# Kernel optimization log

Hardware: AMD Instinct MI355X
Metric: run time of the kernel (lower is better)

## Reference

```python
import jax, jax.numpy as jnp
import numpy as np

NODE_DIM = 128
HIDDEN = 64
N_NODES = 100000
N_REL = 50
N_EDGES = 1000000
TEMPERATURE = 0.5
BIAS = 1e-4


def _xavier(key, shape):
    fan_in, fan_out = shape[0], shape[1]
    lim = jnp.sqrt(6.0 / (fan_in + fan_out))
    return jax.random.uniform(key, shape, jnp.float32, -lim, lim)


def setup_inputs() -> dict:
    key = jax.random.key(0)
    ks = jax.random.split(key, 16)
    inp = {
        "edge_index": jax.random.randint(ks[0], (2, N_EDGES), 0, N_NODES),
        "edge_type": jax.random.randint(ks[1], (N_EDGES,), 0, N_REL),
        "all_embed": jax.random.normal(ks[2], (N_NODES, NODE_DIM), jnp.float32),
        "relation_emb": jax.random.normal(ks[3], (N_REL, NODE_DIM), jnp.float32),
        "u": jax.random.uniform(ks[4], (N_EDGES,), jnp.float32),
    }
    # four 2-layer MLPs: Linear(node_dim, hidden) -> ReLU -> Linear(hidden, 1)
    names = ["src", "dst", "edge", "con"]
    for i, nm in enumerate(names):
        k1, k2 = jax.random.split(ks[5 + i])
        inp[f"W1_{nm}"] = _xavier(k1, (NODE_DIM, HIDDEN))
        inp[f"b1_{nm}"] = jnp.zeros((HIDDEN,), jnp.float32)
        inp[f"W2_{nm}"] = _xavier(k2, (HIDDEN, 1))
        inp[f"b2_{nm}"] = jnp.zeros((1,), jnp.float32)
    return inp


def _mlp(x, W1, b1, W2, b2):
    # x: [E, node_dim] -> [E, 1]
    h = jnp.maximum(x @ W1 + b1, 0.0)
    return h @ W2 + b2


def reference(edge_index, edge_type, all_embed, relation_emb, u,
              W1_src, b1_src, W2_src, b2_src,
              W1_dst, b1_dst, W2_dst, b2_dst,
              W1_edge, b1_edge, W2_edge, b2_edge,
              W1_con, b1_con, W2_con, b2_con):
    head = all_embed[edge_index[0]]          # [E, D] gather
    tail = all_embed[edge_index[1]]          # [E, D] gather
    latent = relation_emb[edge_type]         # [E, D] gather

    weight = _mlp(head + tail + latent, W1_con, b1_con, W2_con, b2_con)
    weight = weight + _mlp(head, W1_src, b1_src, W2_src, b2_src)
    weight = weight + _mlp(tail, W1_dst, b1_dst, W2_dst, b2_dst)
    weight = weight + _mlp(latent, W1_edge, b1_edge, W2_edge, b2_edge)
    weight = weight[:, 0]                    # squeeze -> [E]

    # eps = (bias - (1-bias)) * u + (1-bias), bias = 1e-4
    eps = (2.0 * BIAS - 1.0) * u + (1.0 - BIAS)
    gate_inputs = jnp.log(eps) - jnp.log1p(-eps)
    gate_inputs = (gate_inputs + weight) / TEMPERATURE
    return jax.nn.sigmoid(gate_inputs)       # [E]
```

## Files before the change

### kernel.cpp

```cpp
#include <hip/hip_runtime.h>
#include <hip/hip_bf16.h>
#include <hip/hip_fp16.h>
#include <math.h>

#define NODE_DIM 128
#define HIDDEN   64
#define N_NODES  100000
#define N_RELS   50
#define N_EDGESC 1000000
#define TEMPERATURE 0.5f
#define BIASF 0.0001f
#define NBLK_GEMM ((N_NODES + 127) / 128)

typedef __attribute__((ext_vector_type(8))) _Float16 f16x8;
typedef __attribute__((ext_vector_type(2))) _Float16 hv2;
typedef __attribute__((ext_vector_type(4))) float    f32x4;

union U4 { uint4 u; hv2 h[4]; };

__global__ __launch_bounds__(256) void prep_small(
    const float* __restrict__ W1c, const float* __restrict__ W1s,
    const float* __restrict__ W1d,
    _Float16* __restrict__ wt) {
  const int tid = blockIdx.x * 256 + threadIdx.x;
  const int k = tid / 192;
  const int n = tid % 192;
  const float* W = (n < 64) ? W1c : (n < 128) ? W1s : W1d;
  const float v = W[k * HIDDEN + (n & 63)];
  const int ks = k ^ ((n & 7) << 3);
  wt[n * NODE_DIM + ks] = (_Float16)v;
}

__global__ __launch_bounds__(512) void prep_gemm(
    const float* __restrict__ x,
    const _Float16* __restrict__ wt,
    const float* __restrict__ b1s, const float* __restrict__ W2s,
    const float* __restrict__ b2s,
    const float* __restrict__ b1d, const float* __restrict__ W2d,
    const float* __restrict__ b2d,
    const float* __restrict__ rel_emb,
    const float* __restrict__ W1c, const float* __restrict__ b1c,
    const float* __restrict__ W1e, const float* __restrict__ b1e,
    const float* __restrict__ W2e, const float* __restrict__ b2e,
    const float* __restrict__ b2c, const float* __restrict__ W2c,
    __half* __restrict__ pcon,
    float* __restrict__ ssrc, float* __restrict__ sdst,
    _Float16* __restrict__ qh, float* __restrict__ srel,
    _Float16* __restrict__ w2h) {
  const int wv = threadIdx.x >> 6;
  const int l  = threadIdx.x & 63;

  if (blockIdx.x >= NBLK_GEMM) {
    if (blockIdx.x == NBLK_GEMM && threadIdx.x < HIDDEN)
      w2h[threadIdx.x] = (_Float16)W2c[threadIdx.x];
    const int r = (blockIdx.x - NBLK_GEMM) * 8 + wv;
    if (r >= N_RELS) return;
    const float* xr = rel_emb + (size_t)r * NODE_DIM;
    float ac = 0.f, ae = 0.f;
    #pragma unroll 8
    for (int k = 0; k < NODE_DIM; ++k) {
      float xk = xr[k];
      ac = fmaf(xk, W1c[k * HIDDEN + l], ac);
      ae = fmaf(xk, W1e[k * HIDDEN + l], ae);
    }
    qh[r * HIDDEN + l] = (_Float16)(ac + b1c[l]);
    float he = fmaxf(ae + b1e[l], 0.f) * W2e[l];
    #pragma unroll
    for (int off = 32; off > 0; off >>= 1) he += __shfl_xor(he, off);
    if (l == 0) srel[r] = he + b2e[0] + b2c[0];
    return;
  }

  __shared__ _Float16 bl[192 * NODE_DIM];
  const int hi = l >> 4;
  const int c  = l & 15;

  {
    const char* g = (const char*)wt;
    #pragma unroll
    for (int i = 0; i < 6; ++i) {
      const int chunk = (i * 8 + wv) << 10;
      __builtin_amdgcn_global_load_lds(
          (const __attribute__((address_space(1))) void*)(g + chunk + l * 16),
          (__attribute__((address_space(3))) void*)((char*)bl + chunk),
          16, 0, 0);
    }
  }

  const int m0   = blockIdx.x * 128 + wv * 16;
  const int arow = m0 + c;
  const int rowc = arow < N_NODES ? arow : N_NODES - 1;
  const float* xr = x + (size_t)rowc * NODE_DIM + hi * 8;
  f16x8 a[4];
  #pragma unroll
  for (int s = 0; s < 4; ++s) {
    float4 u0 = *(const float4*)(xr + s * 32);
    float4 u1 = *(const float4*)(xr + s * 32 + 4);
    f16x8 av;
    av[0] = (_Float16)u0.x; av[1] = (_Float16)u0.y;
    av[2] = (_Float16)u0.z; av[3] = (_Float16)u0.w;
    av[4] = (_Float16)u1.x; av[5] = (_Float16)u1.y;
    av[6] = (_Float16)u1.z; av[7] = (_Float16)u1.w;
    a[s] = av;
  }

  __syncthreads();

  f32x4 acc[12];
  #pragma unroll
  for (int i = 0; i < 12; ++i) acc[i] = (f32x4){0.f, 0.f, 0.f, 0.f};

  #pragma unroll
  for (int tt = 0; tt < 12; ++tt) {
    const int n = tt * 16 + c;
    const int nbase = n * NODE_DIM;
    #pragma unroll
    for (int s = 0; s < 4; ++s) {
      const int ks = (s * 32 + hi * 8) ^ ((n & 7) << 3);
      f16x8 b = *(const f16x8*)(&bl[nbase + ks]);
      acc[tt] = __builtin_amdgcn_mfma_f32_16x16x32_f16(a[s], b, acc[tt], 0, 0, 0);
    }
  }

  #pragma unroll
  for (int tt = 0; tt < 4; ++tt) {
    #pragma unroll
    for (int g = 0; g < 4; ++g) {
      const int row = m0 + hi * 4 + g;
      if (row < N_NODES)
        pcon[(size_t)row * HIDDEN + tt * 16 + c] = __float2half(acc[tt][g]);
    }
  }
  float ps[4] = {0.f, 0.f, 0.f, 0.f};
  float pd[4] = {0.f, 0.f, 0.f, 0.f};
  #pragma unroll
  for (int tt = 0; tt < 4; ++tt) {
    const int h = tt * 16 + c;
    const float b1sv = b1s[h], w2sv = W2s[h];
    const float b1dv = b1d[h], w2dv = W2d[h];
    #pragma unroll
    for (int g = 0; g < 4; ++g) {
      ps[g] += fmaxf(acc[4 + tt][g] + b1sv, 0.f) * w2sv;
      pd[g] += fmaxf(acc[8 + tt][g] + b1dv, 0.f) * w2dv;
    }
  }
  #pragma unroll
  for (int off = 1; off < 16; off <<= 1) {
    #pragma unroll
    for (int g = 0; g < 4; ++g) {
      ps[g] += __shfl_xor(ps[g], off);
      pd[g] += __shfl_xor(pd[g], off);
    }
  }
  if (c == 0) {
    const float bs = b2s[0], bd = b2d[0];
    #pragma unroll
    for (int g = 0; g < 4; ++g) {
      const int row = m0 + hi * 4 + g;
      if (row < N_NODES) { ssrc[row] = ps[g] + bs; sdst[row] = pd[g] + bd; }
    }
  }
}

__global__ __launch_bounds__(256) void edge_kernel(
    const int*   __restrict__ edge_index,
    const int*   __restrict__ edge_type,
    const float* __restrict__ u,
    const _Float16* __restrict__ pcon,
    const float* __restrict__ ssrc,
    const float* __restrict__ sdst,
    const _Float16* __restrict__ qh,
    const float* __restrict__ srel,
    const _Float16* __restrict__ w2h,
    float* __restrict__ out) {
  const int tid = blockIdx.x * 256 + threadIdx.x;
  const int e   = tid >> 2;
  const int sub = tid & 3;

  const int src = edge_index[e];
  const int dst = edge_index[N_EDGESC + e];
  const int r   = edge_type[e];

  const uint4* Sp = (const uint4*)(pcon + src * HIDDEN);
  const uint4* Dp = (const uint4*)(pcon + dst * HIDDEN);
  const uint4* Qp = (const uint4*)(qh + r * HIDDEN);
  const uint4* Wp = (const uint4*)w2h;

  U4 s0, s1, d0, d1, q0, q1, w0, w1;
  s0.u = Sp[sub];     s1.u = Sp[sub + 4];
  d0.u = Dp[sub];     d1.u = Dp[sub + 4];
  q0.u = Qp[sub];     q1.u = Qp[sub + 4];
  w0.u = Wp[sub];     w1.u = Wp[sub + 4];
  const float sadd = ssrc[src] + sdst[dst] + srel[r];

  float acc = 0.f;
  #pragma unroll
  for (int j = 0; j < 4; ++j) {
    hv2 h0 = s0.h[j] + d0.h[j] + q0.h[j];
    h0 = __builtin_elementwise_max(h0, (hv2)(_Float16)0.f);
    acc = __builtin_amdgcn_fdot2(h0, w0.h[j], acc, false);
    hv2 h1 = s1.h[j] + d1.h[j] + q1.h[j];
    h1 = __builtin_elementwise_max(h1, (hv2)(_Float16)0.f);
    acc = __builtin_amdgcn_fdot2(h1, w1.h[j], acc, false);
  }
  acc += __shfl_xor(acc, 1);
  acc += __shfl_xor(acc, 2);

  if (sub == 0) {
    const float uu   = u[e];
    const float wsum = acc + sadd;
    const float eps  = fmaf(2.f * BIASF - 1.f, uu, 1.f - BIASF);
    const float ome  = fmaf(1.f - 2.f * BIASF, uu, BIASF);
    const float g    = __logf(eps) - __logf(ome);
    const float z    = (g + wsum) * (1.f / TEMPERATURE);
    out[e] = __builtin_amdgcn_rcpf(1.f + __expf(-z));
  }
}

extern "C" void kernel_launch(void* const* d_in, const int* in_sizes, int n_in,
                              void* d_out, int out_size, void* d_ws, size_t ws_size,
                              hipStream_t stream) {
  const int*   edge_index = (const int*)d_in[0];
  const int*   edge_type  = (const int*)d_in[1];
  const float* all_embed  = (const float*)d_in[2];
  const float* rel_emb    = (const float*)d_in[3];
  const float* u          = (const float*)d_in[4];
  const float* W1_src = (const float*)d_in[5];
  const float* b1_src = (const float*)d_in[6];
  const float* W2_src = (const float*)d_in[7];
  const float* b2_src = (const float*)d_in[8];
  const float* W1_dst = (const float*)d_in[9];
  const float* b1_dst = (const float*)d_in[10];
  const float* W2_dst = (const float*)d_in[11];
  const float* b2_dst = (const float*)d_in[12];
  const float* W1_edge = (const float*)d_in[13];
  const float* b1_edge = (const float*)d_in[14];
  const float* W2_edge = (const float*)d_in[15];
  const float* b2_edge = (const float*)d_in[16];
  const float* W1_con = (const float*)d_in[17];
  const float* b1_con = (const float*)d_in[18];
  const float* W2_con = (const float*)d_in[19];
  const float* b2_con = (const float*)d_in[20];

  char* ws = (char*)d_ws;
  _Float16* pcon = (_Float16*)ws;
  float*    ssrc = (float*)(ws + (size_t)N_NODES * HIDDEN * 2);
  float*    sdst = ssrc + N_NODES;
  _Float16* wt   = (_Float16*)(sdst + N_NODES);
  _Float16* qh   = wt + 192 * NODE_DIM;
  _Float16* w2h  = qh + N_RELS * HIDDEN;
  float*    srel = (float*)(w2h + HIDDEN);

  prep_small<<<96, 256, 0, stream>>>(W1_con, W1_src, W1_dst, wt);

  const int relblk = (N_RELS + 7) / 8;
  prep_gemm<<<NBLK_GEMM + relblk, 512, 0, stream>>>(
      all_embed, wt,
      b1_src, W2_src, b2_src, b1_dst, W2_dst, b2_dst,
      rel_emb, W1_con, b1_con, W1_edge, b1_edge, W2_edge, b2_edge,
      b2_con, W2_con,
      (__half*)pcon, ssrc, sdst, qh, srel, w2h);

  edge_kernel<<<(N_EDGESC * 4) / 256, 256, 0, stream>>>(
      edge_index, edge_type, u, pcon, ssrc, sdst, qh, srel, w2h,
      (float*)d_out);
}
```

Before: 64.67 us.

## Fuse weight transpose into GEMM kernel and use nontemporal streaming loads

Measured after the change: 73.97 us. +14.4%, slower.

```diff
diff --git a/kernel.cpp b/kernel.cpp
--- a/kernel.cpp
+++ b/kernel.cpp
@@ -15,31 +15,20 @@
 typedef __attribute__((ext_vector_type(8))) _Float16 f16x8;
 typedef __attribute__((ext_vector_type(2))) _Float16 hv2;
 typedef __attribute__((ext_vector_type(4))) float    f32x4;
+typedef __attribute__((ext_vector_type(4))) float    f4v;
 
 union U4 { uint4 u; hv2 h[4]; };
-
-__global__ __launch_bounds__(256) void prep_small(
-    const float* __restrict__ W1c, const float* __restrict__ W1s,
-    const float* __restrict__ W1d,
-    _Float16* __restrict__ wt) {
-  const int tid = blockIdx.x * 256 + threadIdx.x;
-  const int k = tid / 192;
-  const int n = tid % 192;
-  const float* W = (n < 64) ? W1c : (n < 128) ? W1s : W1d;
-  const float v = W[k * HIDDEN + (n & 63)];
-  const int ks = k ^ ((n & 7) << 3);
-  wt[n * NODE_DIM + ks] = (_Float16)v;
-}
 
 __global__ __launch_bounds__(512) void prep_gemm(
     const float* __restrict__ x,
-    const _Float16* __restrict__ wt,
+    const float* __restrict__ W1cc, const float* __restrict__ W1ss,
+    const float* __restrict__ W1dd,
     const float* __restrict__ b1s, const float* __restrict__ W2s,
     const float* __restrict__ b2s,
     const float* __restrict__ b1d, const float* __restrict__ W2d,
     const float* __restrict__ b2d,
     const float* __restrict__ rel_emb,
-    const float* __restrict__ W1c, const float* __restrict__ b1c,
+    const float* __restrict__ b1c,
     const float* __restrict__ W1e, const float* __restrict__ b1e,
     const float* __restrict__ W2e, const float* __restrict__ b2e,
     const float* __restrict__ b2c, const float* __restrict__ W2c,
@@ -60,7 +49,7 @@
     #pragma unroll 8
     for (int k = 0; k < NODE_DIM; ++k) {
       float xk = xr[k];
-      ac = fmaf(xk, W1c[k * HIDDEN + l], ac);
+      ac = fmaf(xk, W1cc[k * HIDDEN + l], ac);
       ae = fmaf(xk, W1e[k * HIDDEN + l], ae);
     }
     qh[r * HIDDEN + l] = (_Float16)(ac + b1c[l]);
@@ -75,16 +64,14 @@
   const int hi = l >> 4;
   const int c  = l & 15;
 
-  {
-    const char* g = (const char*)wt;
-    #pragma unroll
-    for (int i = 0; i < 6; ++i) {
-      const int chunk = (i * 8 + wv) << 10;
-      __builtin_amdgcn_global_load_lds(
-          (const __attribute__((address_space(1))) void*)(g + chunk + l * 16),
-          (__attribute__((address_space(3))) void*)((char*)bl + chunk),
-          16, 0, 0);
-    }
+  #pragma unroll 4
+  for (int j = 0; j < 48; ++j) {
+    const int idx = j * 512 + threadIdx.x;
+    const int k = idx / 192;
+    const int n = idx - k * 192;
+    const float* W = (n < 64) ? W1cc : (n < 128) ? W1ss : W1dd;
+    const float v = W[k * HIDDEN + (n & 63)];
+    bl[n * NODE_DIM + (k ^ ((n & 7) << 3))] = (_Float16)v;
   }
 
   const int m0   = blockIdx.x * 128 + wv * 16;
@@ -94,13 +81,13 @@
   f16x8 a[4];
   #pragma unroll
   for (int s = 0; s < 4; ++s) {
-    float4 u0 = *(const float4*)(xr + s * 32);
-    float4 u1 = *(const float4*)(xr + s * 32 + 4);
+    f4v u0 = __builtin_nontemporal_load((const f4v*)(xr + s * 32));
+    f4v u1 = __builtin_nontemporal_load((const f4v*)(xr + s * 32 + 4));
     f16x8 av;
-    av[0] = (_Float16)u0.x; av[1] = (_Float16)u0.y;
-    av[2] = (_Float16)u0.z; av[3] = (_Float16)u0.w;
-    av[4] = (_Float16)u1.x; av[5] = (_Float16)u1.y;
-    av[6] = (_Float16)u1.z; av[7] = (_Float16)u1.w;
+    av[0] = (_Float16)u0[0]; av[1] = (_Float16)u0[1];
+    av[2] = (_Float16)u0[2]; av[3] = (_Float16)u0[3];
+    av[4] = (_Float16)u1[0]; av[5] = (_Float16)u1[1];
+    av[6] = (_Float16)u1[2]; av[7] = (_Float16)u1[3];
     a[s] = av;
   }
 
@@ -177,9 +164,9 @@
   const int e   = tid >> 2;
   const int sub = tid & 3;
 
-  const int src = edge_index[e];
-  const int dst = edge_index[N_EDGESC + e];
-  const int r   = edge_type[e];
+  const int src = __builtin_nontemporal_load(edge_index + e);
+  const int dst = __builtin_nontemporal_load(edge_index + N_EDGESC + e);
+  const int r   = __builtin_nontemporal_load(edge_type + e);
 
   const uint4* Sp = (const uint4*)(pcon + src * HIDDEN);
   const uint4* Dp = (const uint4*)(pcon + dst * HIDDEN);
@@ -207,13 +194,14 @@
   acc += __shfl_xor(acc, 2);
 
   if (sub == 0) {
-    const float uu   = u[e];
+    const float uu   = __builtin_nontemporal_load(u + e);
     const float wsum = acc + sadd;
     const float eps  = fmaf(2.f * BIASF - 1.f, uu, 1.f - BIASF);
     const float ome  = fmaf(1.f - 2.f * BIASF, uu, BIASF);
     const float g    = __logf(eps) - __logf(ome);
     const float z    = (g + wsum) * (1.f / TEMPERATURE);
-    out[e] = __builtin_amdgcn_rcpf(1.f + __expf(-z));
+    const float res  = __builtin_amdgcn_rcpf(1.f + __expf(-z));
+    __builtin_nontemporal_store(res, out + e);
   }
 }
 
@@ -246,18 +234,16 @@
   _Float16* pcon = (_Float16*)ws;
   float*    ssrc = (float*)(ws + (size_t)N_NODES * HIDDEN * 2);
   float*    sdst = ssrc + N_NODES;
-  _Float16* wt   = (_Float16*)(sdst + N_NODES);
-  _Float16* qh   = wt + 192 * NODE_DIM;
+  _Float16* qh   = (_Float16*)(sdst + N_NODES);
   _Float16* w2h  = qh + N_RELS * HIDDEN;
   float*    srel = (float*)(w2h + HIDDEN);
 
-  prep_small<<<96, 256, 0, stream>>>(W1_con, W1_src, W1_dst, wt);
-
   const int relblk = (N_RELS + 7) / 8;
   prep_gemm<<<NBLK_GEMM + relblk, 512, 0, stream>>>(
-      all_embed, wt,
+      all_embed,
+      W1_con, W1_src, W1_dst,
       b1_src, W2_src, b2_src, b1_dst, W2_dst, b2_dst,
-      rel_emb, W1_con, b1_con, W1_edge, b1_edge, W2_edge, b2_edge,
+      rel_emb, b1_con, W1_edge, b1_edge, W2_edge, b2_edge,
       b2_con, W2_con,
       (__half*)pcon, ssrc, sdst, qh, srel, w2h);
 
```
